# Kernel tuning notes

Measured on AMD Instinct MI355X. Metric: run time of the kernel, lower is better.

Reference implementation:

```python
import itertools
import jax, jax.numpy as jnp
import numpy as np

N_FEATURES = 32
DEGREE = 3
BATCH = 32768


def poly_feature_indices(n_features: int, degree: int):
    indices = []
    for d in range(1, degree + 1):
        for combo in itertools.combinations_with_replacement(range(n_features), d):
            indices.append(combo)
    return indices


def padded_index_matrix(n_features: int, degree: int) -> np.ndarray:
    # Pad each monomial index tuple to length `degree` with the sentinel
    # index n_features, which points at a column of ones appended to x.
    idx_list = poly_feature_indices(n_features, degree)
    mat = np.full((len(idx_list), degree), n_features, dtype=np.int32)
    for i, tup in enumerate(idx_list):
        mat[i, : len(tup)] = tup
    return mat


def setup_inputs() -> dict:
    key = jax.random.key(0)
    k1, k2, k3 = jax.random.split(key, 3)
    n_poly = len(poly_feature_indices(N_FEATURES, DEGREE))  # 6544
    x = jax.random.normal(k1, (BATCH, N_FEATURES), dtype=jnp.float32)
    # nn.Linear(n_poly, 1) init scale
    bound = 1.0 / np.sqrt(n_poly)
    W = jax.random.uniform(k2, (1, n_poly), dtype=jnp.float32, minval=-bound, maxval=bound)
    b = jax.random.uniform(k3, (1,), dtype=jnp.float32, minval=-bound, maxval=bound)
    idx = jnp.asarray(padded_index_matrix(N_FEATURES, DEGREE))  # (n_poly, degree) int32
    return {"x": x, "W": W, "b": b, "idx": idx}


def reference(x, W, b, idx):
    # Append a ones column so the sentinel index acts as multiplicative identity.
    x_aug = jnp.concatenate([x, jnp.ones((x.shape[0], 1), dtype=x.dtype)], axis=1)
    # z[b, p] = prod_k x_aug[b, idx[p, k]]  -> (batch, n_poly)
    z = x_aug[:, idx[:, 0]]
    for k in range(1, idx.shape[1]):  # small fixed loop over degree
        z = z * x_aug[:, idx[:, k]]
    # Linear(n_poly, 1): z @ W.T + b
    return z @ W.T + b
```

## Files before the change

kernel.cpp:

```cpp
#include <hip/hip_runtime.h>


__device__ __forceinline__ constexpr int off2(int a, int b) {
    return 32 + 32 * a - (a * (a - 1)) / 2 + (b - a);
}

__device__ __forceinline__ constexpr int off3(int a, int b, int c) {
    constexpr int g3[32] = {
        0,    528,  1024, 1489, 1924, 2330, 2708, 3059,
        3384, 3684, 3960, 4213, 4444, 4654, 4844, 5015,
        5168, 5304, 5424, 5529, 5620, 5698, 5764, 5819,
        5864, 5900, 5928, 5949, 5964, 5974, 5980, 5983};
    return 560 + g3[a] + 32 * (b - a) - ((b * (b - 1)) / 2 - (a * (a - 1)) / 2) + (c - b);
}

template <int A0, int A1>
__device__ __forceinline__ float eval_range(const float* __restrict__ W,
                                            const float (&x)[32]) {
    float acc = 0.0f;
#pragma unroll
    for (int a = A0; a < A1; ++a) {
        const float xa = x[a];
        acc = __builtin_fmaf(W[a], xa, acc);
#pragma unroll
        for (int b = a; b < 32; ++b) {
            const float pab = xa * x[b];
            float S = W[off2(a, b)];
#pragma unroll
            for (int c = b; c < 32; ++c) {
                S = __builtin_fmaf(W[off3(a, b, c)], x[c], S);
            }
            acc = __builtin_fmaf(pab, S, acc);
        }
    }
    return acc;
}

__global__ __launch_bounds__(256) void PolyLinear_40218073760341_kernel(
    const float* __restrict__ X,
    const float* __restrict__ W,
    const float* __restrict__ Bp,
    float* __restrict__ out)
{
    const int lane = threadIdx.x & 63;
    const int wave = threadIdx.x >> 6;
    const int row  = blockIdx.x * 64 + lane;

    float x[32];
    const float4* xr = (const float4*)(X + (long)row * 32);
#pragma unroll
    for (int i = 0; i < 8; ++i) {
        const float4 v = xr[i];
        x[4 * i + 0] = v.x;
        x[4 * i + 1] = v.y;
        x[4 * i + 2] = v.z;
        x[4 * i + 3] = v.w;
    }

    float acc;
    if (wave == 0)      acc = eval_range<0, 3>(W, x);
    else if (wave == 1) acc = eval_range<3, 7>(W, x);
    else if (wave == 2) acc = eval_range<7, 12>(W, x);
    else                acc = eval_range<12, 32>(W, x);

    __shared__ float partial[4][64];
    partial[wave][lane] = acc;
    __syncthreads();

    if (wave == 0) {
        const float r = partial[0][lane] + partial[1][lane] +
                        partial[2][lane] + partial[3][lane] + Bp[0];
        out[row] = r;
    }
}

extern "C" void kernel_launch(void* const* d_in, const int* in_sizes, int n_in,
                              void* d_out, int out_size, void* d_ws, size_t ws_size,
                              hipStream_t stream) {
    const float* X  = (const float*)d_in[0];
    const float* W  = (const float*)d_in[1];
    const float* Bp = (const float*)d_in[2];
    float* out = (float*)d_out;

    const int rows = in_sizes[0] / 32;
    const int grid = rows / 64;
    PolyLinear_40218073760341_kernel<<<grid, 256, 0, stream>>>(X, W, Bp, out);
}
```

Baseline: 82.45 us.

## Recast cubic polynomial contraction as bf16 MFMA over (a,b) pair tiles

The scalar per-thread cubic FMA loops are replaced by a matrix formulation. For each (a,b) pair, a bf16 MFMA 32x32x16 computes the inner sum over c of W*x_c, plus the pair and linear terms, for 32 rows at a time. An epilogue then multiplies by x_a*x_b and reduces across waves. A prep kernel repacks W and the bias into a bf16 tiled layout in workspace on every call. This moves most of the FLOPs onto matrix cores, at the cost of bf16 precision loss in W and x and an extra launch.

```diff
diff --git a/kernel.cpp b/kernel.cpp
--- a/kernel.cpp
+++ b/kernel.cpp
@@ -1,12 +1,18 @@
 #include <hip/hip_runtime.h>
 
 
-__device__ __forceinline__ constexpr int off2(int a, int b) {
+typedef __attribute__((ext_vector_type(8))) short short8;
+typedef __attribute__((ext_vector_type(16))) float f32x16;
+
+#define NT 18
+#define WT_ELEMS (NT * 3 * 2 * 32 * 8)
+
+__host__ __device__ constexpr int off2(int a, int b) {
     return 32 + 32 * a - (a * (a - 1)) / 2 + (b - a);
 }
 
-__device__ __forceinline__ constexpr int off3(int a, int b, int c) {
-    constexpr int g3[32] = {
+__device__ inline int off3_rt(int a, int b, int c) {
+    const int g3[32] = {
         0,    528,  1024, 1489, 1924, 2330, 2708, 3059,
         3384, 3684, 3960, 4213, 4444, 4654, 4844, 5015,
         5168, 5304, 5424, 5529, 5620, 5698, 5764, 5819,
@@ -14,63 +20,139 @@
     return 560 + g3[a] + 32 * (b - a) - ((b * (b - 1)) / 2 - (a * (a - 1)) / 2) + (c - b);
 }
 
-template <int A0, int A1>
-__device__ __forceinline__ float eval_range(const float* __restrict__ W,
-                                            const float (&x)[32]) {
-    float acc = 0.0f;
-#pragma unroll
-    for (int a = A0; a < A1; ++a) {
-        const float xa = x[a];
-        acc = __builtin_fmaf(W[a], xa, acc);
-#pragma unroll
-        for (int b = a; b < 32; ++b) {
-            const float pab = xa * x[b];
-            float S = W[off2(a, b)];
-#pragma unroll
-            for (int c = b; c < 32; ++c) {
-                S = __builtin_fmaf(W[off3(a, b, c)], x[c], S);
+__host__ __device__ constexpr int cpa(int p) {
+    int a = 0, rem = p;
+    while (rem >= 33 - a) { rem -= 33 - a; a++; }
+    return a;
+}
+__host__ __device__ constexpr int cpb(int p) {
+    int a = 0, rem = p;
+    while (rem >= 33 - a) { rem -= 33 - a; a++; }
+    return a + rem;
+}
+
+__device__ inline unsigned short f2bf(float f) {
+    union { float f; unsigned u; } v;
+    v.f = f;
+    unsigned u = v.u + (0x7FFFu + ((v.u >> 16) & 1u));
+    return (unsigned short)(u >> 16);
+}
+
+__global__ __launch_bounds__(256) void prep_wt(const float* __restrict__ W,
+                                               const float* __restrict__ Bp,
+                                               unsigned short* __restrict__ wt) {
+    int e = blockIdx.x * 256 + threadIdx.x;
+    if (e >= WT_ELEMS) return;
+    int j = e % 8, e2 = e / 8;
+    int m = e2 % 32; e2 /= 32;
+    int h = e2 % 2;  e2 /= 2;
+    int kc = e2 % 3; e2 /= 3;
+    int t = e2;
+    int p = t * 32 + m;
+    int c = kc * 16 + h * 8 + j;
+    float v = 0.0f;
+    if (p < 561 && c <= 32) {
+        int a = 0, rem = p;
+        while (rem >= 33 - a) { rem -= 33 - a; a++; }
+        int b = a + rem;
+        if (c >= b) {
+            if (c == 32) {
+                if (b == 32) v = (a == 32) ? Bp[0] : W[a];
+                else         v = W[off2(a, b)];
+            } else {
+                v = W[off3_rt(a, b, c)];
             }
-            acc = __builtin_fmaf(pab, S, acc);
         }
     }
-    return acc;
+    wt[e] = f2bf(v);
+}
+
+template <int T, int H, int R>
+__device__ __forceinline__ void epi(const float (&x)[33], const f32x16& c, float& racc) {
+    if constexpr (R < 16) {
+        constexpr int p = T * 32 + (R & 3) + 8 * (R >> 2) + 4 * H;
+        if constexpr (p < 561) {
+            constexpr int a = cpa(p);
+            constexpr int b = cpb(p);
+            racc = __builtin_fmaf(x[a] * x[b], c[R], racc);
+        }
+        epi<T, H, R + 1>(x, c, racc);
+    }
+}
+
+template <int T>
+__device__ __forceinline__ void tile(const unsigned short* __restrict__ wtl,
+                                     const float (&x)[33],
+                                     const short8& b0, const short8& b1, const short8& b2,
+                                     float& racc, int h) {
+    short8 a0 = *(const short8*)(wtl + (T * 3 + 0) * 512);
+    short8 a1 = *(const short8*)(wtl + (T * 3 + 1) * 512);
+    short8 a2 = *(const short8*)(wtl + (T * 3 + 2) * 512);
+    f32x16 c = {0.0f, 0.0f, 0.0f, 0.0f, 0.0f, 0.0f, 0.0f, 0.0f,
+                0.0f, 0.0f, 0.0f, 0.0f, 0.0f, 0.0f, 0.0f, 0.0f};
+    c = __builtin_amdgcn_mfma_f32_32x32x16_bf16(a0, b0, c, 0, 0, 0);
+    c = __builtin_amdgcn_mfma_f32_32x32x16_bf16(a1, b1, c, 0, 0, 0);
+    c = __builtin_amdgcn_mfma_f32_32x32x16_bf16(a2, b2, c, 0, 0, 0);
+    if (h == 0) epi<T, 0, 0>(x, c, racc);
+    else        epi<T, 1, 0>(x, c, racc);
+}
+
+template <int T0, int T1>
+__device__ __forceinline__ void tiles(const unsigned short* __restrict__ wtl,
+                                      const float (&x)[33],
+                                      const short8& b0, const short8& b1, const short8& b2,
+                                      float& racc, int h) {
+    if constexpr (T0 < T1) {
+        tile<T0>(wtl, x, b0, b1, b2, racc, h);
+        tiles<T0 + 1, T1>(wtl, x, b0, b1, b2, racc, h);
+    }
 }
 
 __global__ __launch_bounds__(256) void PolyLinear_40218073760341_kernel(
-    const float* __restrict__ X,
-    const float* __restrict__ W,
-    const float* __restrict__ Bp,
-    float* __restrict__ out)
-{
-    const int lane = threadIdx.x & 63;
-    const int wave = threadIdx.x >> 6;
-    const int row  = blockIdx.x * 64 + lane;
+    const float* __restrict__ X, const unsigned short* __restrict__ wt,
+    float* __restrict__ out) {
+    const int tid  = threadIdx.x;
+    const int lane = tid & 63;
+    const int wave = tid >> 6;
+    const int h    = (tid >> 5) & 1;
+    const int col  = tid & 31;
+    const long row = (long)blockIdx.x * 32 + col;
 
-    float x[32];
-    const float4* xr = (const float4*)(X + (long)row * 32);
+    float x[33];
+    const float4* xr = (const float4*)(X + row * 32);
 #pragma unroll
     for (int i = 0; i < 8; ++i) {
-        const float4 v = xr[i];
-        x[4 * i + 0] = v.x;
-        x[4 * i + 1] = v.y;
-        x[4 * i + 2] = v.z;
-        x[4 * i + 3] = v.w;
+        float4 v = xr[i];
+        x[4 * i + 0] = v.x; x[4 * i + 1] = v.y;
+        x[4 * i + 2] = v.z; x[4 * i + 3] = v.w;
     }
+    x[32] = 1.0f;
 
-    float acc;
-    if (wave == 0)      acc = eval_range<0, 3>(W, x);
-    else if (wave == 1) acc = eval_range<3, 7>(W, x);
-    else if (wave == 2) acc = eval_range<7, 12>(W, x);
-    else                acc = eval_range<12, 32>(W, x);
+    short8 b0, b1, b2;
+#pragma unroll
+    for (int j = 0; j < 8; ++j) {
+        b0[j] = (short)f2bf(h ? x[8 + j]  : x[j]);
+        b1[j] = (short)f2bf(h ? x[24 + j] : x[16 + j]);
+        b2[j] = 0;
+    }
+    b2[0] = h ? (short)0 : (short)0x3F80;
 
-    __shared__ float partial[4][64];
-    partial[wave][lane] = acc;
+    const unsigned short* wtl = wt + lane * 8;
+
+    float racc = 0.0f;
+    if (wave == 0)      tiles<0, 5>(wtl, x, b0, b1, b2, racc, h);
+    else if (wave == 1) tiles<5, 9>(wtl, x, b0, b1, b2, racc, h);
+    else if (wave == 2) tiles<9, 14>(wtl, x, b0, b1, b2, racc, h);
+    else                tiles<14, 18>(wtl, x, b0, b1, b2, racc, h);
+
+    __shared__ float red[256];
+    red[tid] = racc;
     __syncthreads();
-
-    if (wave == 0) {
-        const float r = partial[0][lane] + partial[1][lane] +
-                        partial[2][lane] + partial[3][lane] + Bp[0];
-        out[row] = r;
+    if (tid < 32) {
+        float s = 0.0f;
+#pragma unroll
+        for (int k = 0; k < 8; ++k) s += red[k * 32 + tid];
+        out[(long)blockIdx.x * 32 + tid] = s;
     }
 }
 
@@ -81,8 +163,10 @@
     const float* W  = (const float*)d_in[1];
     const float* Bp = (const float*)d_in[2];
     float* out = (float*)d_out;
+    unsigned short* wt = (unsigned short*)d_ws;
+
+    prep_wt<<<(WT_ELEMS + 255) / 256, 256, 0, stream>>>(W, Bp, wt);
 
     const int rows = in_sizes[0] / 32;
-    const int grid = rows / 64;
-    PolyLinear_40218073760341_kernel<<<grid, 256, 0, stream>>>(X, W, Bp, out);
+    PolyLinear_40218073760341_kernel<<<rows / 32, 256, 0, stream>>>(X, wt, out);
 }
```

After: 83.85 us. No clear change (+1.7%).
